# Performance work log

Hardware: AMD Instinct MI355X
Metric: run time of the kernel (lower is better)

The kernel has to match this reference:

```python
import jax, jax.numpy as jnp
import numpy as np

B, N, HS, NH = 32, 256, 768, 32
D = HS // NH  # 24


def setup_inputs() -> dict:
    key = jax.random.key(0)
    ks = jax.random.split(key, 20)
    s = 0.02
    inp = {
        "hidden_states": jax.random.normal(ks[0], (B, N, HS), jnp.float32),
        "attention_bias": jax.random.normal(ks[1], (B, NH, N, N), jnp.float32),
        "delta_pos": jax.random.normal(ks[2], (B, N, N, 3), jnp.float32),
        "attention_mask": jnp.ones((B, N), jnp.float32),
        "Wi": jax.random.normal(ks[3], (HS, HS), jnp.float32) * s,
        "bi": jnp.zeros((HS,), jnp.float32),
        "Wq": jax.random.normal(ks[4], (HS, HS), jnp.float32) * s,
        "bq": jnp.zeros((HS,), jnp.float32),
        "Wk": jax.random.normal(ks[5], (HS, HS), jnp.float32) * s,
        "bk": jnp.zeros((HS,), jnp.float32),
        "Wv": jax.random.normal(ks[6], (HS, HS), jnp.float32) * s,
        "bv": jnp.zeros((HS,), jnp.float32),
        "Wf1": jax.random.normal(ks[7], (1, HS), jnp.float32) * s,
        "bf1": jnp.zeros((1,), jnp.float32),
        "Wf2": jax.random.normal(ks[8], (1, HS), jnp.float32) * s,
        "bf2": jnp.zeros((1,), jnp.float32),
        "Wf3": jax.random.normal(ks[9], (1, HS), jnp.float32) * s,
        "bf3": jnp.zeros((1,), jnp.float32),
    }
    return inp


def reference(hidden_states, attention_bias, delta_pos, attention_mask,
              Wi, bi, Wq, bq, Wk, bk, Wv, bv, Wf1, bf1, Wf2, bf2, Wf3, bf3):
    b, n, hs = hidden_states.shape
    nh = NH
    d = hs // nh
    denoise_scaling = d ** (-0.5)
    scale = np.sqrt(denoise_scaling).astype(np.float32)

    # mask: (B,N) -> additive (B,1,1,N)
    neg = ((1.0 - attention_mask) * -100000.0)[:, None, None, :]

    h = jax.nn.gelu(hidden_states @ Wi.T + bi, approximate=False)
    q = (h @ Wq.T + bq).reshape(b, n, nh, d).transpose(0, 2, 1, 3) * scale
    k = (h @ Wk.T + bk).reshape(b, n, nh, d).transpose(0, 2, 1, 3) * scale
    v = (h @ Wv.T + bv).reshape(b, n, nh, d).transpose(0, 2, 1, 3)

    scores = jnp.einsum('bhid,bhjd->bhij', q, k) + attention_bias + neg
    probs = jax.nn.softmax(scores, axis=-1)  # dropout = identity at eval

    # x[b,i,c,h,d] = sum_j probs[b,h,i,j] * delta_pos[b,i,j,c] * v[b,h,j,d]
    x = jnp.einsum('bhij,bijc,bhjd->bichd', probs, delta_pos, v)
    x = x.reshape(b, n, 3, hs)

    f1 = x[:, :, 0, :] @ Wf1.T + bf1  # (B,N,1)
    f2 = x[:, :, 1, :] @ Wf2.T + bf2
    f3 = x[:, :, 2, :] @ Wf3.T + bf3
    return jnp.concatenate([f1, f2, f3], axis=-1).astype(jnp.float32)
```

## Files before the change

### kernel.cpp

```cpp
#include <hip/hip_runtime.h>
#include <hip/hip_fp16.h>

#define B_  32
#define N_  256
#define HS_ 768
#define NH_ 32
#define D_  24
#define M_  (B_*N_)
#define NQKU 1664

typedef unsigned short us8 __attribute__((ext_vector_type(8)));
typedef unsigned short us4v __attribute__((ext_vector_type(4)));
typedef _Float16 f16x8 __attribute__((ext_vector_type(8)));
typedef float f32x4 __attribute__((ext_vector_type(4)));

__device__ __forceinline__ unsigned short f2h(float x){
  return __half_as_ushort(__float2half(x));
}
__device__ __forceinline__ float h2f(unsigned short u){
  return __half2float(__ushort_as_half(u));
}
__device__ __forceinline__ void gload16(const void* g, void* l){
  __builtin_amdgcn_global_load_lds(
      (const __attribute__((address_space(1))) void*)g,
      (__attribute__((address_space(3))) void*)l, 16, 0, 0);
}
__device__ __forceinline__ void pin4(float4 &v){
  asm volatile("" : "+v"(v.x), "+v"(v.y), "+v"(v.z), "+v"(v.w));
}
__device__ __forceinline__ float fexp2(float x){
  float r; asm("v_exp_f32 %0, %1" : "=v"(r) : "v"(x)); return r;
}
__device__ __forceinline__ float red32(float v, int hi){
  float a = v, b = v;
  asm("v_permlane32_swap_b32 %0, %1" : "+v"(a), "+v"(b));
  return v + (hi ? a : b);
}

__global__ __launch_bounds__(256) void cvt_kernel(const float* __restrict__ in,
                                                  unsigned short* __restrict__ out, int n4){
  int i = blockIdx.x*256 + threadIdx.x;
  if (i >= n4) return;
  float4 v = ((const float4*)in)[i];
  ushort4 o;
  o.x = f2h(v.x); o.y = f2h(v.y); o.z = f2h(v.z); o.w = f2h(v.w);
  ((ushort4*)out)[i] = o;
}

__global__ __launch_bounds__(256) void wuprep_kernel(
    const float* __restrict__ Wv, const float* __restrict__ bvv,
    const float* __restrict__ Wf1, const float* __restrict__ Wf2, const float* __restrict__ Wf3,
    unsigned short* __restrict__ wu,
    float* __restrict__ bu)
{
  int r = blockIdx.x;
  unsigned short* dst = wu + (size_t)r*768;
  int k = threadIdx.x;
  if (r < 96){
    int c = r >> 5, h = r & 31;
    const float* wf = (c == 0 ? Wf1 : c == 1 ? Wf2 : Wf3) + h*D_;
    float wfl[24];
#pragma unroll
    for (int d = 0; d < 24; d++) wfl[d] = wf[d];
    for (int kk = k; kk < 768; kk += 256){
      float s = 0.f;
#pragma unroll
      for (int d = 0; d < 24; d++) s += wfl[d]*Wv[(size_t)(h*24 + d)*768 + kk];
      dst[kk] = f2h(s);
    }
    if (k == 0){
      float s = 0.f;
      for (int d = 0; d < 24; d++) s += bvv[h*24 + d]*wfl[d];
      bu[r] = s;
    }
  } else {
    for (int kk = k; kk < 768; kk += 256) dst[kk] = 0;
    if (k == 0) bu[r] = 0.f;
  }
}

__global__ __launch_bounds__(256) void gemm128_kernel(
    const unsigned short* __restrict__ A, const unsigned short* __restrict__ W,
    const float* __restrict__ b0, const float* __restrict__ b1, const float* __restrict__ b2,
    unsigned short* __restrict__ C, unsigned short* __restrict__ qkvh,
    unsigned short* __restrict__ u16,
    int M, int N, int K, int dogelu, int mode)
{
  __shared__ unsigned short As[128*64];
  __shared__ unsigned short Bs[128*64];
  int gswz = blockIdx.x;
  int chunkg = gridDim.x >> 3;
  int bid = (gswz & 7)*chunkg + (gswz >> 3);
  int tid = threadIdx.x;
  int nT = N >> 7;
  int tm = bid / nT;
  int tn = bid - tm*nT;
  int wave = tid >> 6, lane = tid & 63;
  int wm = (wave >> 1) << 6;
  int wn = (wave & 1) << 6;
  int fr = lane & 15;
  int g  = lane >> 4;

  size_t aoff[4], woff[4];
  int ldsb[4];
#pragma unroll
  for (int s4 = 0; s4 < 4; s4++){
    int ob = s4*4096 + tid*16;
    int r  = ob >> 7;
    int p  = (ob >> 4) & 7;
    int l  = p ^ (r & 7);
    aoff[s4] = ((size_t)(tm*128 + r)*K)*2 + l*16;
    woff[s4] = ((size_t)(tn*128 + r)*K)*2 + l*16;
    ldsb[s4] = s4*4096 + wave*1024;
  }
  const char* Ab = (const char*)A;
  const char* Wb = (const char*)W;
  char* AsB = (char*)As;
  char* BsB = (char*)Bs;

  f32x4 acc[4][4];
#pragma unroll
  for (int m = 0; m < 4; m++)
#pragma unroll
    for (int n = 0; n < 4; n++) acc[m][n] = (f32x4){0.f,0.f,0.f,0.f};

  for (int k0 = 0; k0 < K; k0 += 64){
    size_t kb = (size_t)k0*2;
#pragma unroll
    for (int s4 = 0; s4 < 4; s4++) gload16(Ab + aoff[s4] + kb, AsB + ldsb[s4]);
#pragma unroll
    for (int s4 = 0; s4 < 4; s4++) gload16(Wb + woff[s4] + kb, BsB + ldsb[s4]);
    __syncthreads();

    f16x8 af[4], bf[4];
#pragma unroll
    for (int m = 0; m < 4; m++){
      int row = wm + m*16 + fr;
      af[m] = __builtin_bit_cast(f16x8, *(const us8*)(AsB + row*128 + ((g ^ (row & 7))*16)));
    }
#pragma unroll
    for (int n = 0; n < 4; n++){
      int row = wn + n*16 + fr;
      bf[n] = __builtin_bit_cast(f16x8, *(const us8*)(BsB + row*128 + ((g ^ (row & 7))*16)));
    }
#pragma unroll
    for (int m = 0; m < 4; m++)
#pragma unroll
      for (int n = 0; n < 4; n++)
        acc[m][n] = __builtin_amdgcn_mfma_f32_16x16x32_f16(af[m], bf[n], acc[m][n], 0, 0, 0);

#pragma unroll
    for (int m = 0; m < 4; m++){
      int row = wm + m*16 + fr;
      af[m] = __builtin_bit_cast(f16x8, *(const us8*)(AsB + row*128 + (((g+4) ^ (row & 7))*16)));
    }
#pragma unroll
    for (int n = 0; n < 4; n++){
      int row = wn + n*16 + fr;
      bf[n] = __builtin_bit_cast(f16x8, *(const us8*)(BsB + row*128 + (((g+4) ^ (row & 7))*16)));
    }
#pragma unroll
    for (int m = 0; m < 4; m++)
#pragma unroll
      for (int n = 0; n < 4; n++)
        acc[m][n] = __builtin_amdgcn_mfma_f32_16x16x32_f16(af[m], bf[n], acc[m][n], 0, 0, 0);
    __syncthreads();
  }

  if (mode == 0){
    const float* bp = b0;
#pragma unroll
    for (int n = 0; n < 4; n++){
      int col = tn*128 + wn + n*16 + fr;
      float bv = bp[col];
#pragma unroll
      for (int m = 0; m < 4; m++){
        int row = tm*128 + wm + m*16 + g*4;
#pragma unroll
        for (int q = 0; q < 4; q++){
          float v = acc[m][n][q] + bv;
          if (dogelu) v = 0.5f*v*(1.0f + erff(v*0.70710678118654752f));
          C[(size_t)(row + q)*N + col] = f2h(v);
        }
      }
    }
  } else {
    int which = (tn < 6) ? 0 : (tn < 12) ? 1 : 2;
    if (which < 2){
      const float* bp = which ? (b1 - 768) : b0;
#pragma unroll
      for (int n = 0; n < 4; n++){
        int col = tn*128 + wn + n*16 + fr;
        float bv = bp[col];
        int hd = col - which*768;
        int hh = hd / 24;
        int dd = hd - hh*24;
#pragma unroll
        for (int m = 0; m < 4; m++){
          int row = tm*128 + wm + m*16 + g*4;
          size_t hmbase = ((size_t)(which*1024 + (row >> 8)*32 + hh))*6144 + (row & 255)*24 + dd;
#pragma unroll
          for (int q = 0; q < 4; q++)
            qkvh[hmbase + q*24] = f2h(acc[m][n][q] + bv);
        }
      }
    } else {
#pragma unroll
      for (int n = 0; n < 4; n++){
        int col = tn*128 + wn + n*16 + fr;
        int cu = col - 1536;
        if (cu < 96){
          int c = cu >> 5, hh = cu & 31;
          float bv = b2[cu];
#pragma unroll
          for (int m = 0; m < 4; m++){
            int row = tm*128 + wm + m*16 + g*4;
            int bb = row >> 8, nr = row & 255;
            unsigned short* ud = u16 + ((size_t)(bb*32 + hh)*256 + nr)*4 + c;
#pragma unroll
            for (int q = 0; q < 4; q++)
              ud[q*4] = f2h(acc[m][n][q] + bv);
          }
        }
      }
    }
  }
}

#define SCALE 0.20412414523193154f
#define INVSCALE 4.898979485566356f
#define SL2 0.2944888918959693f
#define ML2 -23.083120654223414f
#define NEGS (100000.0f*INVSCALE)
__global__ __launch_bounds__(256, 4) void attn_kernel(
    const unsigned short* __restrict__ qkvh,
    const float* __restrict__ bias,
    const unsigned short* __restrict__ u16,
    const float* __restrict__ mask,
    const float* __restrict__ dp,
    float* __restrict__ fpart)
{
  int gswz = blockIdx.x;
  int lin = (gswz & 7)*128 + (gswz >> 3);
  int b = lin >> 5, ic = (lin >> 1) & 15, jh = lin & 1;
  int i0 = ic*16, j00 = jh*128;
  int t = threadIdx.x;
  int wave = t >> 6, lane = t & 63;
  int ch = wave, fr = lane & 15, g = lane >> 4;
  int hi32 = lane & 32;

  __shared__ __align__(16) char smem[35840];
  char* zp = smem + 32768;
  char* scratch = smem + 33792;

  int bsrc[2];
#pragma unroll
  for (int k = 0; k < 2; k++){
    int a = k*4096 + t*16;
    int row = a >> 9;
    int pc = (a >> 4) & 31;
    int lc = pc ^ (row & 7);
    bsrc[k] = row*1024 + lc*16;
  }
  const char* bb0 = (const char*)bias
      + ((size_t)(b*NH_)*65536 + (size_t)i0*256 + j00)*4;

  const char* qkvhB = (const char*)qkvh;
  const char* kbase0 = qkvhB + ((size_t)(1024 + b*32))*12288 + jh*6144;
  const char* qbase0 = qkvhB + ((size_t)(b*32))*12288 + (size_t)i0*48;
  const char* ubase0 = (const char*)u16 + ((size_t)(b*NH_))*2048 + jh*1024;
  const char* sbase[2]; size_t sstep[2];
#pragma unroll
  for (int k = 0; k < 2; k++){
    int G = k*256 + t;
    if (G < 384){ sbase[k] = kbase0 + G*16;            sstep[k] = 12288; }
    else if (G < 432){ sbase[k] = qbase0 + (G-384)*16; sstep[k] = 12288; }
    else if (G < 496){ sbase[k] = ubase0 + (G-432)*16; sstep[k] = 2048; }
    else { sbase[k] = ubase0; sstep[k] = 2048; }
  }

  #define ISSUE(hh) do { \
    int _par = (hh) & 1; \
    const char* _bp = bb0 + (size_t)(hh)*262144; \
    gload16(_bp + bsrc[0], smem + _par*8192 + wave*1024); \
    gload16(_bp + bsrc[1], smem + _par*8192 + 4096 + wave*1024); \
    gload16(sbase[0] + (size_t)(hh)*sstep[0], smem + 16384 + _par*8192 + wave*1024); \
    gload16(sbase[1] + (size_t)(hh)*sstep[1], smem + 16384 + _par*8192 + 4096 + wave*1024); \
  } while(0)

  float4 nvs[2]; float4 dpre[6];
  {
    const float* mb = mask + b*N_ + j00;
#pragma unroll
    for (int jt = 0; jt < 2; jt++){
      float4 m4 = *(const float4*)(mb + ch*32 + jt*16 + g*4);
      nvs[jt].x = fmaf(m4.x, NEGS, -NEGS);
      nvs[jt].y = fmaf(m4.y, NEGS, -NEGS);
      nvs[jt].z = fmaf(m4.z, NEGS, -NEGS);
      nvs[jt].w = fmaf(m4.w, NEGS, -NEGS);
    }
    const float* dpb = dp + (size_t)(b*N_ + i0 + fr)*768;
#pragma unroll
    for (int jt = 0; jt < 2; jt++){
      const float4* dq = (const float4*)(dpb + (size_t)(j00 + ch*32 + jt*16 + g*4)*3);
      dpre[jt*3+0] = dq[0]; dpre[jt*3+1] = dq[1]; dpre[jt*3+2] = dq[2];
    }
  }
  asm volatile("s_waitcnt vmcnt(0)" ::: "memory");
  pin4(nvs[0]); pin4(nvs[1]);
#pragma unroll
  for (int k = 0; k < 6; k++) pin4(dpre[k]);

  ISSUE(0);
  gload16(mask + b*N_, scratch);
  if (t < 128) *(us8*)(zp + t*16) = (us8){0,0,0,0,0,0,0,0};
  asm volatile("s_waitcnt lgkmcnt(0)" ::: "memory");

  int swz = (fr & 7) << 4;
  float4* fp4 = (float4*)fpart;
  size_t fbase = (((size_t)(b*16 + ic)*2 + jh)*32)*64 + ch*16 + fr;

#pragma unroll 1
  for (int h = 0; h < 32; h++){
    asm volatile("s_waitcnt vmcnt(1)" ::: "memory");
    __builtin_amdgcn_s_barrier();
    if (h < 31) ISSUE(h+1);

    const char* bslot = smem + (h & 1)*8192;
    const char* sslot = smem + 16384 + (h & 1)*8192;

    const char* qa = (g < 3) ? (sslot + 6144 + fr*48 + g*16) : (zp + fr*16);
    f16x8 qf = __builtin_bit_cast(f16x8, *(const us8*)qa);

    float S = 0.f, a0 = 0.f, a1 = 0.f, a2 = 0.f;
#pragma unroll
    for (int jt = 0; jt < 2; jt++){
      int j0l = ch*32 + jt*16 + g*4;
      float4 bv = *(const float4*)(bslot + fr*512 + ((j0l*4) ^ swz));
      f32x4 cin;
      cin[0] = fmaf(bv.x, INVSCALE, nvs[jt].x);
      cin[1] = fmaf(bv.y, INVSCALE, nvs[jt].y);
      cin[2] = fmaf(bv.z, INVSCALE, nvs[jt].z);
      cin[3] = fmaf(bv.w, INVSCALE, nvs[jt].w);
      int krow = ch*32 + jt*16 + fr;
      const char* ka = sslot + krow*48 + g*16;
      f16x8 kf = __builtin_bit_cast(f16x8, *(const us8*)ka);
      f32x4 sv = __builtin_amdgcn_mfma_f32_16x16x32_f16(kf, qf, cin, 0, 0, 0);
      float p0 = fexp2(fmaf(sv[0], SL2, ML2));
      float p1 = fexp2(fmaf(sv[1], SL2, ML2));
      float p2 = fexp2(fmaf(sv[2], SL2, ML2));
      float p3 = fexp2(fmaf(sv[3], SL2, ML2));
      S += p0 + p1 + p2 + p3;
      us8 ua = *(const us8*)(sslot + 6912 + j0l*8);
      us8 ub = *(const us8*)(sslot + 6912 + j0l*8 + 16);
      float4 d0 = dpre[jt*3], d1 = dpre[jt*3+1], d2 = dpre[jt*3+2];
      a0 += p0*h2f(ua[0])*d0.x + p1*h2f(ua[4])*d0.w + p2*h2f(ub[0])*d1.z + p3*h2f(ub[4])*d2.y;
      a1 += p0*h2f(ua[1])*d0.y + p1*h2f(ua[5])*d1.x + p2*h2f(ub[1])*d1.w + p3*h2f(ub[5])*d2.z;
      a2 += p0*h2f(ua[2])*d0.z + p1*h2f(ua[6])*d1.y + p2*h2f(ub[2])*d2.x + p3*h2f(ub[6])*d2.w;
    }
    S  += __shfl_xor(S, 16);   S  = red32(S, hi32);
    a0 += __shfl_xor(a0, 16);  a0 = red32(a0, hi32);
    a1 += __shfl_xor(a1, 16);  a1 = red32(a1, hi32);
    a2 += __shfl_xor(a2, 16);  a2 = red32(a2, hi32);
    if (lane < 16)
      fp4[fbase + (size_t)h*64] = make_float4(S, a0, a1, a2);
  }
  asm volatile("s_waitcnt vmcnt(0)" ::: "memory");
  #undef ISSUE
}

__global__ __launch_bounds__(256) void final_kernel(const float* __restrict__ fpart,
    const float* __restrict__ bf1, const float* __restrict__ bf2, const float* __restrict__ bf3,
    float* __restrict__ out)
{
  int idx = blockIdx.x*256 + threadIdx.x;
  int b = idx >> 8, i = idx & 255;
  int ic = i >> 4, ii = i & 15;
  const float4* fp4 = (const float4*)fpart;
  size_t base = ((size_t)(b*16 + ic)*2)*2048 + ii;
  float acc0 = 0.f, acc1 = 0.f, acc2 = 0.f;
#pragma unroll 4
  for (int h = 0; h < 32; h++){
    float S = 0.f, A0 = 0.f, A1 = 0.f, A2 = 0.f;
#pragma unroll
    for (int jh = 0; jh < 2; jh++){
#pragma unroll
      for (int ch = 0; ch < 4; ch++){
        float4 v = fp4[base + (size_t)jh*2048 + (size_t)h*64 + ch*16];
        S += v.x; A0 += v.y; A1 += v.z; A2 += v.w;
      }
    }
    float rs = 1.0f / S;
    acc0 += A0*rs; acc1 += A1*rs; acc2 += A2*rs;
  }
  float* op = out + (size_t)idx*3;
  op[0] = acc0 + bf1[0];
  op[1] = acc1 + bf2[0];
  op[2] = acc2 + bf3[0];
}

extern "C" void kernel_launch(void* const* d_in, const int* in_sizes, int n_in,
                              void* d_out, int out_size, void* d_ws, size_t ws_size,
                              hipStream_t stream)
{
  const float* X    = (const float*)d_in[0];
  const float* bias = (const float*)d_in[1];
  const float* dp   = (const float*)d_in[2];
  const float* mask = (const float*)d_in[3];
  const float* Wi   = (const float*)d_in[4];
  const float* bi   = (const float*)d_in[5];
  const float* Wq   = (const float*)d_in[6];
  const float* bq   = (const float*)d_in[7];
  const float* Wk   = (const float*)d_in[8];
  const float* bk   = (const float*)d_in[9];
  const float* Wv   = (const float*)d_in[10];
  const float* bv   = (const float*)d_in[11];
  const float* Wf1  = (const float*)d_in[12];
  const float* bf1  = (const float*)d_in[13];
  const float* Wf2  = (const float*)d_in[14];
  const float* bf2  = (const float*)d_in[15];
  const float* Wf3  = (const float*)d_in[16];
  const float* bf3  = (const float*)d_in[17];
  float* out = (float*)d_out;

  unsigned short* xb   = (unsigned short*)d_ws;
  unsigned short* wib  = xb   + (size_t)M_*HS_;
  unsigned short* wqk  = wib  + (size_t)HS_*HS_;
  unsigned short* hb   = wqk  + (size_t)NQKU*HS_;
  unsigned short* qkvh = hb   + (size_t)M_*HS_;
  unsigned short* u16a = qkvh + (size_t)2*1024*6144;
  float* bu    = (float*)(u16a + (size_t)B_*NH_*N_*4);
  float* fpart = bu + 128;

  {
    int n4 = M_*HS_/4;
    cvt_kernel<<<n4/256, 256, 0, stream>>>(X, xb, n4);
    int w4 = HS_*HS_/4;
    cvt_kernel<<<w4/256, 256, 0, stream>>>(Wi, wib, w4);
    cvt_kernel<<<w4/256, 256, 0, stream>>>(Wq, wqk, w4);
    cvt_kernel<<<w4/256, 256, 0, stream>>>(Wk, wqk + (size_t)768*768, w4);
    wuprep_kernel<<<128, 256, 0, stream>>>(Wv, bv, Wf1, Wf2, Wf3,
                                           wqk + (size_t)1536*768, bu);
  }

  gemm128_kernel<<<(M_/128)*(HS_/128), 256, 0, stream>>>(
      xb, wib, bi, bi, bi, hb, hb, u16a, M_, HS_, HS_, 1, 0);
  gemm128_kernel<<<(M_/128)*(NQKU/128), 256, 0, stream>>>(
      hb, wqk, bq, bk, bu, hb, qkvh, u16a, M_, NQKU, HS_, 0, 1);

  attn_kernel<<<B_*16*2, 256, 0, stream>>>(qkvh, bias, u16a, mask, dp, fpart);

  final_kernel<<<(B_*N_)/256, 256, 0, stream>>>(fpart, bf1, bf2, bf3, out);
}
```

Before: 180.1 us.

## Triple-buffer attention bias loads with two-head prefetch depth

The attention kernel now keeps three LDS slots for the per-head bias tile and prefetches bias two heads ahead, while the K/Q/U side data stays double-buffered one head ahead. A small zero buffer is written to global memory by the weight-prep kernel and loaded into the side slot, replacing the LDS zeroing and the unused mask scratch load. This targets the main memory-bound cost, the bias stream, by keeping more loads in flight. In exchange, LDS use grows to 40 KB per block, which may limit occupancy, and the loop now issues redundant loads past the last head using index wraparound.

```diff
diff --git a/kernel.cpp b/kernel.cpp
--- a/kernel.cpp
+++ b/kernel.cpp
@@ -51,11 +51,13 @@
     const float* __restrict__ Wv, const float* __restrict__ bvv,
     const float* __restrict__ Wf1, const float* __restrict__ Wf2, const float* __restrict__ Wf3,
     unsigned short* __restrict__ wu,
-    float* __restrict__ bu)
+    float* __restrict__ bu,
+    unsigned short* __restrict__ zws)
 {
   int r = blockIdx.x;
   unsigned short* dst = wu + (size_t)r*768;
   int k = threadIdx.x;
+  if (r == 0 && k < 16) ((us8*)zws)[k] = (us8){0,0,0,0,0,0,0,0};
   if (r < 96){
     int c = r >> 5, h = r & 31;
     const float* wf = (c == 0 ? Wf1 : c == 1 ? Wf2 : Wf3) + h*D_;
@@ -238,6 +240,7 @@
     const unsigned short* __restrict__ u16,
     const float* __restrict__ mask,
     const float* __restrict__ dp,
+    const unsigned short* __restrict__ zws,
     float* __restrict__ fpart)
 {
   int gswz = blockIdx.x;
@@ -249,9 +252,7 @@
   int ch = wave, fr = lane & 15, g = lane >> 4;
   int hi32 = lane & 32;
 
-  __shared__ __align__(16) char smem[35840];
-  char* zp = smem + 32768;
-  char* scratch = smem + 33792;
+  __shared__ __align__(16) char smem[40960];
 
   int bsrc[2];
 #pragma unroll
@@ -276,16 +277,18 @@
     if (G < 384){ sbase[k] = kbase0 + G*16;            sstep[k] = 12288; }
     else if (G < 432){ sbase[k] = qbase0 + (G-384)*16; sstep[k] = 12288; }
     else if (G < 496){ sbase[k] = ubase0 + (G-432)*16; sstep[k] = 2048; }
-    else { sbase[k] = ubase0; sstep[k] = 2048; }
-  }
-
-  #define ISSUE(hh) do { \
+    else { sbase[k] = (const char*)zws + (G-496)*16;   sstep[k] = 0; }
+  }
+
+  #define ISSUE_BIAS(hh, slot) do { \
+    const char* _bp = bb0 + (size_t)((hh) & 31)*262144; \
+    gload16(_bp + bsrc[0], smem + (slot)*8192 + wave*1024); \
+    gload16(_bp + bsrc[1], smem + (slot)*8192 + 4096 + wave*1024); \
+  } while(0)
+  #define ISSUE_SIDE(hh) do { \
     int _par = (hh) & 1; \
-    const char* _bp = bb0 + (size_t)(hh)*262144; \
-    gload16(_bp + bsrc[0], smem + _par*8192 + wave*1024); \
-    gload16(_bp + bsrc[1], smem + _par*8192 + 4096 + wave*1024); \
-    gload16(sbase[0] + (size_t)(hh)*sstep[0], smem + 16384 + _par*8192 + wave*1024); \
-    gload16(sbase[1] + (size_t)(hh)*sstep[1], smem + 16384 + _par*8192 + 4096 + wave*1024); \
+    gload16(sbase[0] + (size_t)((hh) & 31)*sstep[0], smem + 24576 + _par*8192 + wave*1024); \
+    gload16(sbase[1] + (size_t)((hh) & 31)*sstep[1], smem + 24576 + _par*8192 + 4096 + wave*1024); \
   } while(0)
 
   float4 nvs[2]; float4 dpre[6];
@@ -311,10 +314,11 @@
 #pragma unroll
   for (int k = 0; k < 6; k++) pin4(dpre[k]);
 
-  ISSUE(0);
-  gload16(mask + b*N_, scratch);
-  if (t < 128) *(us8*)(zp + t*16) = (us8){0,0,0,0,0,0,0,0};
-  asm volatile("s_waitcnt lgkmcnt(0)" ::: "memory");
+  ISSUE_BIAS(0, 0);
+  ISSUE_SIDE(0);
+  ISSUE_BIAS(1, 1);
+  gload16(zws, smem + 16384);
+  asm volatile("s_waitcnt vmcnt(2)" ::: "memory");
 
   int swz = (fr & 7) << 4;
   float4* fp4 = (float4*)fpart;
@@ -322,12 +326,18 @@
 
 #pragma unroll 1
   for (int h = 0; h < 32; h++){
-    asm volatile("s_waitcnt vmcnt(1)" ::: "memory");
+    asm volatile("s_waitcnt vmcnt(3)" ::: "memory");
     __builtin_amdgcn_s_barrier();
-    if (h < 31) ISSUE(h+1);
-
-    const char* bslot = smem + (h & 1)*8192;
-    const char* sslot = smem + 16384 + (h & 1)*8192;
+    ISSUE_SIDE(h + 1);
+    {
+      int s2 = (h + 2) % 3;
+      ISSUE_BIAS(h + 2, s2);
+    }
+    __builtin_amdgcn_sched_barrier(0);
+
+    const char* bslot = smem + (h % 3)*8192;
+    const char* sslot = smem + 24576 + (h & 1)*8192;
+    const char* zp = sslot + 7936;
 
     const char* qa = (g < 3) ? (sslot + 6144 + fr*48 + g*16) : (zp + fr*16);
     f16x8 qf = __builtin_bit_cast(f16x8, *(const us8*)qa);
@@ -366,7 +376,8 @@
       fp4[fbase + (size_t)h*64] = make_float4(S, a0, a1, a2);
   }
   asm volatile("s_waitcnt vmcnt(0)" ::: "memory");
-  #undef ISSUE
+  #undef ISSUE_BIAS
+  #undef ISSUE_SIDE
 }
 
 __global__ __launch_bounds__(256) void final_kernel(const float* __restrict__ fpart,
@@ -430,7 +441,8 @@
   unsigned short* qkvh = hb   + (size_t)M_*HS_;
   unsigned short* u16a = qkvh + (size_t)2*1024*6144;
   float* bu    = (float*)(u16a + (size_t)B_*NH_*N_*4);
-  float* fpart = bu + 128;
+  unsigned short* zws = (unsigned short*)(bu + 128);
+  float* fpart = (float*)(zws + 128);
 
   {
     int n4 = M_*HS_/4;
@@ -440,7 +452,7 @@
     cvt_kernel<<<w4/256, 256, 0, stream>>>(Wq, wqk, w4);
     cvt_kernel<<<w4/256, 256, 0, stream>>>(Wk, wqk + (size_t)768*768, w4);
     wuprep_kernel<<<128, 256, 0, stream>>>(Wv, bv, Wf1, Wf2, Wf3,
-                                           wqk + (size_t)1536*768, bu);
+                                           wqk + (size_t)1536*768, bu, zws);
   }
 
   gemm128_kernel<<<(M_/128)*(HS_/128), 256, 0, stream>>>(
@@ -448,7 +460,7 @@
   gemm128_kernel<<<(M_/128)*(NQKU/128), 256, 0, stream>>>(
       hb, wqk, bq, bk, bu, hb, qkvh, u16a, M_, NQKU, HS_, 0, 1);
 
-  attn_kernel<<<B_*16*2, 256, 0, stream>>>(qkvh, bias, u16a, mask, dp, fpart);
+  attn_kernel<<<B_*16*2, 256, 0, stream>>>(qkvh, bias, u16a, mask, dp, zws, fpart);
 
   final_kernel<<<(B_*N_)/256, 256, 0, stream>>>(fpart, bf1, bf2, bf3, out);
 }
```

New measurement: 181.3 us. About the same (+0.6%).

## Retile attention blocks to 32 query rows by 64 keys per block

Applied to the files above, without the earlier changes.

Each attention block now covers 32 query rows and a quarter of the key range, with waves split into two row groups and two key chunks, instead of 16 rows by half the keys. This changes how much K/V and Q data is staged per block and reuses each key tile across more query rows. The zero padding for the Q fragment now comes from a global zero buffer loaded asynchronously, replacing the LDS zeroing and its wait, which also shrinks shared memory. The final reduction kernel is updated to sum four key partitions, and the partial-sum buffer layout changes to match.

```diff
diff --git a/kernel.cpp b/kernel.cpp
--- a/kernel.cpp
+++ b/kernel.cpp
@@ -51,11 +51,13 @@
     const float* __restrict__ Wv, const float* __restrict__ bvv,
     const float* __restrict__ Wf1, const float* __restrict__ Wf2, const float* __restrict__ Wf3,
     unsigned short* __restrict__ wu,
-    float* __restrict__ bu)
+    float* __restrict__ bu,
+    unsigned short* __restrict__ zws)
 {
   int r = blockIdx.x;
   unsigned short* dst = wu + (size_t)r*768;
   int k = threadIdx.x;
+  if (r == 0 && k < 16) ((us8*)zws)[k] = (us8){0,0,0,0,0,0,0,0};
   if (r < 96){
     int c = r >> 5, h = r & 31;
     const float* wf = (c == 0 ? Wf1 : c == 1 ? Wf2 : Wf3) + h*D_;
@@ -238,27 +240,28 @@
     const unsigned short* __restrict__ u16,
     const float* __restrict__ mask,
     const float* __restrict__ dp,
+    const unsigned short* __restrict__ zws,
     float* __restrict__ fpart)
 {
   int gswz = blockIdx.x;
   int lin = (gswz & 7)*128 + (gswz >> 3);
-  int b = lin >> 5, ic = (lin >> 1) & 15, jh = lin & 1;
-  int i0 = ic*16, j00 = jh*128;
+  int b = lin >> 5, icp = (lin >> 2) & 7, jq = lin & 3;
+  int i0 = icp*32, j00 = jq*64;
   int t = threadIdx.x;
   int wave = t >> 6, lane = t & 63;
-  int ch = wave, fr = lane & 15, g = lane >> 4;
+  int rg = wave >> 1, ch = wave & 1;
+  int fr = lane & 15, g = lane >> 4;
+  int rl = rg*16 + fr;
   int hi32 = lane & 32;
 
-  __shared__ __align__(16) char smem[35840];
-  char* zp = smem + 32768;
-  char* scratch = smem + 33792;
+  __shared__ __align__(16) char smem[32768];
 
   int bsrc[2];
 #pragma unroll
   for (int k = 0; k < 2; k++){
     int a = k*4096 + t*16;
-    int row = a >> 9;
-    int pc = (a >> 4) & 31;
+    int row = a >> 8;
+    int pc = (a >> 4) & 15;
     int lc = pc ^ (row & 7);
     bsrc[k] = row*1024 + lc*16;
   }
@@ -266,17 +269,17 @@
       + ((size_t)(b*NH_)*65536 + (size_t)i0*256 + j00)*4;
 
   const char* qkvhB = (const char*)qkvh;
-  const char* kbase0 = qkvhB + ((size_t)(1024 + b*32))*12288 + jh*6144;
+  const char* kbase0 = qkvhB + ((size_t)(1024 + b*32))*12288 + jq*3072;
   const char* qbase0 = qkvhB + ((size_t)(b*32))*12288 + (size_t)i0*48;
-  const char* ubase0 = (const char*)u16 + ((size_t)(b*NH_))*2048 + jh*1024;
+  const char* ubase0 = (const char*)u16 + ((size_t)(b*NH_))*2048 + jq*512;
   const char* sbase[2]; size_t sstep[2];
 #pragma unroll
   for (int k = 0; k < 2; k++){
     int G = k*256 + t;
-    if (G < 384){ sbase[k] = kbase0 + G*16;            sstep[k] = 12288; }
-    else if (G < 432){ sbase[k] = qbase0 + (G-384)*16; sstep[k] = 12288; }
-    else if (G < 496){ sbase[k] = ubase0 + (G-432)*16; sstep[k] = 2048; }
-    else { sbase[k] = ubase0; sstep[k] = 2048; }
+    if (G < 192){ sbase[k] = kbase0 + G*16;            sstep[k] = 12288; }
+    else if (G < 288){ sbase[k] = qbase0 + (G-192)*16; sstep[k] = 12288; }
+    else if (G < 320){ sbase[k] = ubase0 + (G-288)*16; sstep[k] = 2048; }
+    else { sbase[k] = (const char*)zws + ((G & 15))*16; sstep[k] = 0; }
   }
 
   #define ISSUE(hh) do { \
@@ -299,7 +302,7 @@
       nvs[jt].z = fmaf(m4.z, NEGS, -NEGS);
       nvs[jt].w = fmaf(m4.w, NEGS, -NEGS);
     }
-    const float* dpb = dp + (size_t)(b*N_ + i0 + fr)*768;
+    const float* dpb = dp + (size_t)(b*N_ + i0 + rl)*768;
 #pragma unroll
     for (int jt = 0; jt < 2; jt++){
       const float4* dq = (const float4*)(dpb + (size_t)(j00 + ch*32 + jt*16 + g*4)*3);
@@ -312,13 +315,11 @@
   for (int k = 0; k < 6; k++) pin4(dpre[k]);
 
   ISSUE(0);
-  gload16(mask + b*N_, scratch);
-  if (t < 128) *(us8*)(zp + t*16) = (us8){0,0,0,0,0,0,0,0};
-  asm volatile("s_waitcnt lgkmcnt(0)" ::: "memory");
+  gload16(zws, smem + 16384 + 5376);
 
   int swz = (fr & 7) << 4;
   float4* fp4 = (float4*)fpart;
-  size_t fbase = (((size_t)(b*16 + ic)*2 + jh)*32)*64 + ch*16 + fr;
+  size_t fbase = (size_t)lin*2048 + rl*2 + ch;
 
 #pragma unroll 1
   for (int h = 0; h < 32; h++){
@@ -328,22 +329,23 @@
 
     const char* bslot = smem + (h & 1)*8192;
     const char* sslot = smem + 16384 + (h & 1)*8192;
-
-    const char* qa = (g < 3) ? (sslot + 6144 + fr*48 + g*16) : (zp + fr*16);
+    const char* zp = sslot + 5120;
+
+    const char* qa = (g < 3) ? (sslot + 3072 + rl*48 + g*16) : (zp + fr*16);
     f16x8 qf = __builtin_bit_cast(f16x8, *(const us8*)qa);
 
     float S = 0.f, a0 = 0.f, a1 = 0.f, a2 = 0.f;
 #pragma unroll
     for (int jt = 0; jt < 2; jt++){
       int j0l = ch*32 + jt*16 + g*4;
-      float4 bv = *(const float4*)(bslot + fr*512 + ((j0l*4) ^ swz));
+      float4 bv = *(const float4*)(bslot + rl*256 + ((j0l*4) ^ swz));
       f32x4 cin;
       cin[0] = fmaf(bv.x, INVSCALE, nvs[jt].x);
       cin[1] = fmaf(bv.y, INVSCALE, nvs[jt].y);
       cin[2] = fmaf(bv.z, INVSCALE, nvs[jt].z);
       cin[3] = fmaf(bv.w, INVSCALE, nvs[jt].w);
-      int krow = ch*32 + jt*16 + fr;
-      const char* ka = sslot + krow*48 + g*16;
+      int kj = ch*32 + jt*16 + fr;
+      const char* ka = sslot + kj*48 + g*16;
       f16x8 kf = __builtin_bit_cast(f16x8, *(const us8*)ka);
       f32x4 sv = __builtin_amdgcn_mfma_f32_16x16x32_f16(kf, qf, cin, 0, 0, 0);
       float p0 = fexp2(fmaf(sv[0], SL2, ML2));
@@ -351,8 +353,8 @@
       float p2 = fexp2(fmaf(sv[2], SL2, ML2));
       float p3 = fexp2(fmaf(sv[3], SL2, ML2));
       S += p0 + p1 + p2 + p3;
-      us8 ua = *(const us8*)(sslot + 6912 + j0l*8);
-      us8 ub = *(const us8*)(sslot + 6912 + j0l*8 + 16);
+      us8 ua = *(const us8*)(sslot + 4608 + j0l*8);
+      us8 ub = *(const us8*)(sslot + 4608 + j0l*8 + 16);
       float4 d0 = dpre[jt*3], d1 = dpre[jt*3+1], d2 = dpre[jt*3+2];
       a0 += p0*h2f(ua[0])*d0.x + p1*h2f(ua[4])*d0.w + p2*h2f(ub[0])*d1.z + p3*h2f(ub[4])*d2.y;
       a1 += p0*h2f(ua[1])*d0.y + p1*h2f(ua[5])*d1.x + p2*h2f(ub[1])*d1.w + p3*h2f(ub[5])*d2.z;
@@ -375,18 +377,18 @@
 {
   int idx = blockIdx.x*256 + threadIdx.x;
   int b = idx >> 8, i = idx & 255;
-  int ic = i >> 4, ii = i & 15;
+  int icp = i >> 5, ii = i & 31;
   const float4* fp4 = (const float4*)fpart;
-  size_t base = ((size_t)(b*16 + ic)*2)*2048 + ii;
+  size_t base = ((size_t)(b*8 + icp)*4)*2048 + ii*2;
   float acc0 = 0.f, acc1 = 0.f, acc2 = 0.f;
 #pragma unroll 4
   for (int h = 0; h < 32; h++){
     float S = 0.f, A0 = 0.f, A1 = 0.f, A2 = 0.f;
 #pragma unroll
-    for (int jh = 0; jh < 2; jh++){
-#pragma unroll
-      for (int ch = 0; ch < 4; ch++){
-        float4 v = fp4[base + (size_t)jh*2048 + (size_t)h*64 + ch*16];
+    for (int jq = 0; jq < 4; jq++){
+#pragma unroll
+      for (int ch = 0; ch < 2; ch++){
+        float4 v = fp4[base + (size_t)jq*2048 + (size_t)h*64 + ch];
         S += v.x; A0 += v.y; A1 += v.z; A2 += v.w;
       }
     }
@@ -430,7 +432,8 @@
   unsigned short* qkvh = hb   + (size_t)M_*HS_;
   unsigned short* u16a = qkvh + (size_t)2*1024*6144;
   float* bu    = (float*)(u16a + (size_t)B_*NH_*N_*4);
-  float* fpart = bu + 128;
+  unsigned short* zws = (unsigned short*)(bu + 128);
+  float* fpart = (float*)(zws + 128);
 
   {
     int n4 = M_*HS_/4;
@@ -440,7 +443,7 @@
     cvt_kernel<<<w4/256, 256, 0, stream>>>(Wq, wqk, w4);
     cvt_kernel<<<w4/256, 256, 0, stream>>>(Wk, wqk + (size_t)768*768, w4);
     wuprep_kernel<<<128, 256, 0, stream>>>(Wv, bv, Wf1, Wf2, Wf3,
-                                           wqk + (size_t)1536*768, bu);
+                                           wqk + (size_t)1536*768, bu, zws);
   }
 
   gemm128_kernel<<<(M_/128)*(HS_/128), 256, 0, stream>>>(
@@ -448,7 +451,7 @@
   gemm128_kernel<<<(M_/128)*(NQKU/128), 256, 0, stream>>>(
       hb, wqk, bq, bk, bu, hb, qkvh, u16a, M_, NQKU, HS_, 0, 1);
 
-  attn_kernel<<<B_*16*2, 256, 0, stream>>>(qkvh, bias, u16a, mask, dp, fpart);
+  attn_kernel<<<B_*8*4, 256, 0, stream>>>(qkvh, bias, u16a, mask, dp, zws, fpart);
 
   final_kernel<<<(B_*N_)/256, 256, 0, stream>>>(fpart, bf1, bf2, bf3, out);
 }
```

Measured after the change: 188.7 us. 1.05x slower.
